# Performance work log

Measured on AMD Instinct MI355X. Metric: run time of the kernel, lower is better.

The kernel has to match this reference:

```python
import jax, jax.numpy as jnp
import numpy as np

N_HEAD = 12
D_HEAD = 64  # key_dim // n_head = 768 // 12


def sparsemax(z):
    # Martins & Astudillo (2016): projection of each row of z onto the simplex.
    K = z.shape[-1]
    z_sorted = -jnp.sort(-z, axis=-1)                      # descending sort
    cs = jnp.cumsum(z_sorted, axis=-1)
    r = jnp.arange(1, K + 1, dtype=z.dtype)
    support = (1.0 + r * z_sorted) > cs                    # support set indicator
    ksz = jnp.sum(support, axis=-1, keepdims=True)         # support size k(z)
    cs_k = jnp.take_along_axis(cs, ksz.astype(jnp.int32) - 1, axis=-1)
    tau = (cs_k - 1.0) / ksz.astype(z.dtype)               # threshold
    return jnp.maximum(z - tau, 0.0)


def setup_inputs() -> dict:
    key = jax.random.key(0)
    kq, kk, kv, kwq, kbq, kwk, kbk = jax.random.split(key, 7)
    B, L, D = 8, 1024, 768
    scale = 0.02
    return {
        "q": jax.random.normal(kq, (B, L, D), jnp.float32),
        "k": jax.random.normal(kk, (B, L, D), jnp.float32),
        "v": jax.random.normal(kv, (B, L, D), jnp.float32),
        "Wq": jax.random.normal(kwq, (D, D), jnp.float32) * scale,  # torch Linear weight [out,in]
        "bq": jax.random.normal(kbq, (D,), jnp.float32) * scale,
        "Wk": jax.random.normal(kwk, (D, D), jnp.float32) * scale,
        "bk": jax.random.normal(kbk, (D,), jnp.float32) * scale,
    }


def reference(q, k, v, Wq, bq, Wk, bk):
    B, Lq, _ = q.shape
    Lkv = k.shape[1]
    # project and split heads: [B, H, L, d_head]
    qh = (q @ Wq.T + bq).reshape(B, Lq, N_HEAD, D_HEAD).transpose(0, 2, 1, 3)
    kh = (k @ Wk.T + bk).reshape(B, Lkv, N_HEAD, D_HEAD).transpose(0, 2, 1, 3)
    inv_sqrt_d = jnp.asarray(1.0 / np.sqrt(D_HEAD), q.dtype)
    scores = jnp.einsum("bhqd,bhkd->bhqk", qh, kh) * inv_sqrt_d  # [B,H,Lq,Lkv]
    attn = sparsemax(scores)
    attn = attn.mean(axis=1)                                      # head-mean -> [B,Lq,Lkv]
    # eval mode: smooth_max is identity (training-only smoothing)
    output = jnp.einsum("bqk,bkd->bqd", attn, v)                  # [B,Lq,Dv]
    return output, attn
```

## Files before the change

kernel.cpp:

```cpp
#include <hip/hip_runtime.h>

#define BSZ 8
#define NH 12
#define LSEQ 1024
#define DMODEL 768
#define DHEAD 64
#define OUT_ELEMS 6291456
#define ATTN_ELEMS 8388608

typedef __attribute__((ext_vector_type(8))) short short8;
typedef __attribute__((ext_vector_type(4))) float f32x4;

__device__ __forceinline__ int   f2i(float x) { union { float f; int i; } c; c.f = x; return c.i; }
__device__ __forceinline__ float i2f(int x)   { union { int i; float f; } c; c.i = x; return c.f; }

__device__ __forceinline__ unsigned short f2bf(float x) {
    union { float f; unsigned u; } c; c.f = x;
    unsigned r = (c.u + 0x7FFF + ((c.u >> 16) & 1)) >> 16;
    return (unsigned short)r;
}
__device__ __forceinline__ float bf2f(unsigned short h) {
    union { float f; unsigned u; } c; c.u = ((unsigned)h) << 16;
    return c.f;
}
__device__ __forceinline__ void split2(float x, unsigned short& h, unsigned short& l) {
    h = f2bf(x);
    l = f2bf(x - bf2f(h));
}

template<int CTRL>
__device__ __forceinline__ float dppadd(float v) {
    return v + i2f(__builtin_amdgcn_update_dpp(0, f2i(v), CTRL, 0xF, 0xF, true));
}
template<int CTRL>
__device__ __forceinline__ float dppmax(float v) {
    return fmaxf(v, i2f(__builtin_amdgcn_update_dpp(f2i(v), f2i(v), CTRL, 0xF, 0xF, false)));
}

__device__ __forceinline__ void wsum2(float s[2]) {
#define WS(CTRL) _Pragma("unroll") for (int rr = 0; rr < 2; ++rr) { s[rr] = dppadd<CTRL>(s[rr]); }
    WS(0x111) WS(0x112) WS(0x114) WS(0x118) WS(0x142) WS(0x143)
#undef WS
#pragma unroll
    for (int rr = 0; rr < 2; ++rr) s[rr] = i2f(__builtin_amdgcn_readlane(f2i(s[rr]), 63));
}

__device__ __forceinline__ void wred6(float s[2], float q[2], float m[2]) {
#define WS(CTRL) _Pragma("unroll") for (int rr = 0; rr < 2; ++rr) { s[rr] = dppadd<CTRL>(s[rr]); q[rr] = dppadd<CTRL>(q[rr]); m[rr] = dppmax<CTRL>(m[rr]); }
    WS(0x111) WS(0x112) WS(0x114) WS(0x118) WS(0x142) WS(0x143)
#undef WS
#pragma unroll
    for (int rr = 0; rr < 2; ++rr) {
        s[rr] = i2f(__builtin_amdgcn_readlane(f2i(s[rr]), 63));
        q[rr] = i2f(__builtin_amdgcn_readlane(f2i(q[rr]), 63));
        m[rr] = i2f(__builtin_amdgcn_readlane(f2i(m[rr]), 63));
    }
}

__global__ __launch_bounds__(256) void proj_mfma(
    const float* __restrict__ qin, const float* __restrict__ kin,
    const float* __restrict__ Wq, const float* __restrict__ bq,
    const float* __restrict__ Wk, const float* __restrict__ bk,
    unsigned short* __restrict__ ws) {
    const float* A; const float* W; const float* bias;
    unsigned short* hi; unsigned short* lo;
    if (blockIdx.z == 0) { A = qin; W = Wq; bias = bq; hi = ws;                lo = ws + OUT_ELEMS; }
    else                 { A = kin; W = Wk; bias = bk; hi = ws + 2*OUT_ELEMS; lo = ws + 3*OUT_ELEMS; }

    __shared__ unsigned short Ah[128][32], Al[128][32];
    __shared__ unsigned short Bh[128][32], Bl[128][32];

    const int t    = threadIdx.x;
    const int lane = t & 63;
    const int w    = t >> 6;
    const int wr   = w >> 1, wc = w & 1;
    const int mrow = lane & 15, quad = lane >> 4;
    const int m0   = blockIdx.y * 128;
    const int n0   = blockIdx.x * 128;

    const int srow = t >> 3;
    const int scol = (t & 7) * 4;

    f32x4 acc[4][4];
#pragma unroll
    for (int i = 0; i < 4; ++i)
#pragma unroll
        for (int j = 0; j < 4; ++j) acc[i][j] = (f32x4){0.f, 0.f, 0.f, 0.f};

    for (int k0 = 0; k0 < DMODEL; k0 += 32) {
        float4 av[4], wv[4];
#pragma unroll
        for (int i = 0; i < 4; ++i) {
            av[i] = *(const float4*)&A[(size_t)(m0 + srow + i * 32) * DMODEL + k0 + scol];
            wv[i] = *(const float4*)&W[(size_t)(n0 + srow + i * 32) * DMODEL + k0 + scol];
        }
        __syncthreads();
#pragma unroll
        for (int i = 0; i < 4; ++i) {
            ushort4 h4, l4;
            split2(av[i].x, h4.x, l4.x); split2(av[i].y, h4.y, l4.y);
            split2(av[i].z, h4.z, l4.z); split2(av[i].w, h4.w, l4.w);
            *(ushort4*)&Ah[srow + i * 32][scol] = h4;
            *(ushort4*)&Al[srow + i * 32][scol] = l4;
            split2(wv[i].x, h4.x, l4.x); split2(wv[i].y, h4.y, l4.y);
            split2(wv[i].z, h4.z, l4.z); split2(wv[i].w, h4.w, l4.w);
            *(ushort4*)&Bh[srow + i * 32][scol] = h4;
            *(ushort4*)&Bl[srow + i * 32][scol] = l4;
        }
        __syncthreads();

        short8 ah[4], al[4], bh[4], bl[4];
#pragma unroll
        for (int i = 0; i < 4; ++i) {
            ah[i] = *(const short8*)&Ah[wr * 64 + i * 16 + mrow][quad * 8];
            al[i] = *(const short8*)&Al[wr * 64 + i * 16 + mrow][quad * 8];
            bh[i] = *(const short8*)&Bh[wc * 64 + i * 16 + mrow][quad * 8];
            bl[i] = *(const short8*)&Bl[wc * 64 + i * 16 + mrow][quad * 8];
        }
#pragma unroll
        for (int i = 0; i < 4; ++i)
#pragma unroll
            for (int j = 0; j < 4; ++j) {
                acc[i][j] = __builtin_amdgcn_mfma_f32_16x16x32_bf16(al[i], bh[j], acc[i][j], 0, 0, 0);
                acc[i][j] = __builtin_amdgcn_mfma_f32_16x16x32_bf16(ah[i], bl[j], acc[i][j], 0, 0, 0);
                acc[i][j] = __builtin_amdgcn_mfma_f32_16x16x32_bf16(ah[i], bh[j], acc[i][j], 0, 0, 0);
            }
    }

#pragma unroll
    for (int j = 0; j < 4; ++j) {
        const int ng = n0 + wc * 64 + j * 16 + mrow;
        const float bj = bias[ng];
        const int hh = ng >> 6, dd = ng & 63;
#pragma unroll
        for (int i = 0; i < 4; ++i) {
#pragma unroll
            for (int reg = 0; reg < 4; ++reg) {
                const int mg = m0 + wr * 64 + i * 16 + quad * 4 + reg;
                const float c = acc[i][j][reg] + bj;
                unsigned short ch, cl;
                split2(c, ch, cl);
                const size_t idx = (((size_t)(mg >> 10) * NH + hh) * LSEQ + (mg & 1023)) * DHEAD + dd;
                hi[idx] = ch;
                lo[idx] = cl;
            }
        }
    }
}

__global__ __launch_bounds__(512, 4) void attn_kernel(
    const unsigned short* __restrict__ ws, float* __restrict__ attn_out) {
    __shared__ float S[16 * 1024];

    const unsigned short* Qhi = ws;
    const unsigned short* Qlo = ws + OUT_ELEMS;
    const unsigned short* Khi = ws + 2 * OUT_ELEMS;
    const unsigned short* Klo = ws + 3 * OUT_ELEMS;

    const int t = threadIdx.x;
    const int lane = t & 63;
    const int w = t >> 6;
    const int idlin = blockIdx.x + 64 * blockIdx.y;
    const int b  = idlin & 7;
    const int q0 = (idlin >> 3) * 16;
    const int hoff = ((idlin >> 3) & 1) * 6;

    const int mrow = lane & 15;
    const int quad = lane >> 4;

    float macc[2][16];
#pragma unroll
    for (int rr = 0; rr < 2; ++rr)
#pragma unroll
        for (int j = 0; j < 16; ++j) macc[rr][j] = 0.f;

    size_t hb;
    short8 qh0, qh1, ql0, ql1;
    short8 kah0, kah1, kal0, kal1;
    short8 kbh0, kbh1, kbl0, kbl1;
    short8 kch0, kch1, kcl0, kcl1;

#define QLOAD() do { \
    const size_t aoff_ = hb + (size_t)(q0 + mrow) * DHEAD + quad * 8; \
    qh0 = *(const short8*)(Qhi + aoff_); \
    qh1 = *(const short8*)(Qhi + aoff_ + 32); \
    ql0 = *(const short8*)(Qlo + aoff_); \
    ql1 = *(const short8*)(Qlo + aoff_ + 32); \
} while (0)

#define KLOAD(P, nt) do { \
    const size_t boff_ = hb + (size_t)(w * 128 + (nt) * 16 + mrow) * DHEAD + quad * 8; \
    P##h0 = *(const short8*)(Khi + boff_); \
    P##h1 = *(const short8*)(Khi + boff_ + 32); \
    P##l0 = *(const short8*)(Klo + boff_); \
    P##l1 = *(const short8*)(Klo + boff_ + 32); \
} while (0)

#define KMFMA(P, nt) do { \
    f32x4 d_ = (f32x4){0.f, 0.f, 0.f, 0.f}; \
    d_ = __builtin_amdgcn_mfma_f32_16x16x32_bf16(ql0, P##h0, d_, 0, 0, 0); \
    d_ = __builtin_amdgcn_mfma_f32_16x16x32_bf16(qh0, P##l0, d_, 0, 0, 0); \
    d_ = __builtin_amdgcn_mfma_f32_16x16x32_bf16(qh0, P##h0, d_, 0, 0, 0); \
    d_ = __builtin_amdgcn_mfma_f32_16x16x32_bf16(ql1, P##h1, d_, 0, 0, 0); \
    d_ = __builtin_amdgcn_mfma_f32_16x16x32_bf16(qh1, P##l1, d_, 0, 0, 0); \
    d_ = __builtin_amdgcn_mfma_f32_16x16x32_bf16(qh1, P##h1, d_, 0, 0, 0); \
    const int swcol_ = (w * 128 + (nt) * 16 + mrow) ^ (quad << 4); \
    _Pragma("unroll") for (int reg = 0; reg < 4; ++reg) \
        S[(quad * 4 + reg) * 1024 + swcol_] = d_[reg] * 0.125f; \
} while (0)

#define SP_PASS() do { \
    _Pragma("unroll") for (int rr = 0; rr < 2; ++rr) { \
        float a0 = 0.f, a1 = 0.f, a2 = 0.f, a3 = 0.f; \
        int c = 0; \
        _Pragma("unroll") for (int j = 0; j < 16; j += 4) { \
            bool g0 = z[rr][j]     > tau[rr]; \
            bool g1 = z[rr][j + 1] > tau[rr]; \
            bool g2 = z[rr][j + 2] > tau[rr]; \
            bool g3 = z[rr][j + 3] > tau[rr]; \
            c += __popcll(__ballot(g0)) + __popcll(__ballot(g1)) \
               + __popcll(__ballot(g2)) + __popcll(__ballot(g3)); \
            a0 += g0 ? z[rr][j]     : 0.f; \
            a1 += g1 ? z[rr][j + 1] : 0.f; \
            a2 += g2 ? z[rr][j + 2] : 0.f; \
            a3 += g3 ? z[rr][j + 3] : 0.f; \
        } \
        sI[rr] = (a0 + a1) + (a2 + a3); \
        cI[rr] = c; \
    } \
    wsum2(sI); \
} while (0)

    hb = ((size_t)b * NH + hoff) * (LSEQ * DHEAD);
    QLOAD();

#pragma unroll 1
    for (int i = 0; i < NH; ++i) {
        __syncthreads();

        KLOAD(ka, 0); KLOAD(kb, 1);
        KLOAD(kc, 2); KMFMA(ka, 0);
        KLOAD(ka, 3); KMFMA(kb, 1);
        KLOAD(kb, 4); KMFMA(kc, 2);
        KLOAD(kc, 5); KMFMA(ka, 3);
        KLOAD(ka, 6); KMFMA(kb, 4);
        KLOAD(kb, 7); KMFMA(kc, 5);
        KMFMA(ka, 6); KMFMA(kb, 7);
        __syncthreads();

        float z[2][16];
#pragma unroll
        for (int rr = 0; rr < 2; ++rr) {
            const int r = w * 2 + rr;
            const int swz = (r >> 2) << 4;
#pragma unroll
            for (int c = 0; c < 4; ++c)
                *(f32x4*)&z[rr][c * 4] = *(const f32x4*)&S[r * 1024 + ((c * 256 + lane * 4) ^ swz)];
        }

        if (i + 1 < NH) {
            int hn = i + 1 + hoff; if (hn >= NH) hn -= NH;
            hb = ((size_t)b * NH + hn) * (LSEQ * DHEAD);
            QLOAD();
        }

        float sv[2], qv[2], mv[2];
#pragma unroll
        for (int rr = 0; rr < 2; ++rr) {
            float s0 = 0.f, s1 = 0.f, s2 = 0.f, s3 = 0.f;
            float p0 = 0.f, p1 = 0.f, p2 = 0.f, p3 = 0.f;
            float m0 = z[rr][0], m1 = z[rr][1], m2 = z[rr][2], m3 = z[rr][3];
#pragma unroll
            for (int j = 0; j < 16; j += 4) {
                s0 += z[rr][j]; s1 += z[rr][j + 1]; s2 += z[rr][j + 2]; s3 += z[rr][j + 3];
                p0 = fmaf(z[rr][j],     z[rr][j],     p0);
                p1 = fmaf(z[rr][j + 1], z[rr][j + 1], p1);
                p2 = fmaf(z[rr][j + 2], z[rr][j + 2], p2);
                p3 = fmaf(z[rr][j + 3], z[rr][j + 3], p3);
            }
#pragma unroll
            for (int j = 4; j < 16; j += 4) {
                m0 = fmaxf(m0, z[rr][j]);     m1 = fmaxf(m1, z[rr][j + 1]);
                m2 = fmaxf(m2, z[rr][j + 2]); m3 = fmaxf(m3, z[rr][j + 3]);
            }
            sv[rr] = (s0 + s1) + (s2 + s3);
            qv[rr] = (p0 + p1) + (p2 + p3);
            mv[rr] = fmaxf(fmaxf(m0, m1), fmaxf(m2, m3));
        }
        wred6(sv, qv, mv);

        float tau[2], t0s[2]; int prev[2]; bool done[2];
#pragma unroll
        for (int rr = 0; rr < 2; ++rr) {
            t0s[rr] = fmaxf((sv[rr] - 1.0f) * (1.0f / 1024.0f), mv[rr] - 1.0f);
            const float mu  = sv[rr] * (1.0f / 1024.0f);
            const float var = fmaxf(qv[rr] * (1.0f / 1024.0f) - mu * mu, 1e-12f);
            const float sg  = sqrtf(var);
            const float a   = 2.7196f + 0.33333f * __logf(sg);
            const float tg  = mu + (a - 0.25f) * sg;
            tau[rr] = fminf(fmaxf(tg, t0s[rr]), mv[rr] - 1e-3f);
            prev[rr] = -1; done[rr] = false;
        }

        {
            float sI[2]; int cI[2];
            SP_PASS();
#pragma unroll
            for (int rr = 0; rr < 2; ++rr) {
                const float tn = (sI[rr] - 1.0f) / (float)cI[rr];
                if (tn >= tau[rr]) { tau[rr] = tn; prev[rr] = cI[rr]; }
                else               { tau[rr] = t0s[rr]; }
            }
        }

        for (int it = 0; it < 63; ++it) {
            float sI[2]; int cI[2];
            SP_PASS();
            bool alldone = true;
#pragma unroll
            for (int rr = 0; rr < 2; ++rr) {
                if (!done[rr]) {
                    if (cI[rr] == prev[rr]) done[rr] = true;
                    else { tau[rr] = (sI[rr] - 1.0f) / (float)cI[rr]; prev[rr] = cI[rr]; }
                }
                alldone = alldone && done[rr];
            }
            if (alldone) break;
        }

#pragma unroll
        for (int rr = 0; rr < 2; ++rr)
#pragma unroll
            for (int j = 0; j < 16; ++j)
                macc[rr][j] += fmaxf(z[rr][j] - tau[rr], 0.f);
    }

    float* ao = attn_out + ((size_t)b * LSEQ + q0) * LSEQ;
#pragma unroll
    for (int rr = 0; rr < 2; ++rr) {
        const int r = w * 2 + rr;
#pragma unroll
        for (int c = 0; c < 4; ++c) {
            f32x4 o;
#pragma unroll
            for (int j = 0; j < 4; ++j) o[j] = macc[rr][c * 4 + j] * (1.0f / 12.0f);
            *(f32x4*)&ao[(size_t)r * LSEQ + c * 256 + lane * 4] = o;
        }
    }
#undef QLOAD
#undef KLOAD
#undef KMFMA
#undef SP_PASS
}

__global__ __launch_bounds__(256) void out_mfma(
    const float* __restrict__ attn, const float* __restrict__ v,
    float* __restrict__ out) {
    const int b = blockIdx.z;
    const float* Ab = attn + (size_t)b * LSEQ * LSEQ;
    const float* Vb = v    + (size_t)b * LSEQ * DMODEL;
    float* Cb       = out  + (size_t)b * LSEQ * DMODEL;

    __shared__ unsigned short Ah[128][32], Al[128][32];
    __shared__ unsigned short Bh[128][36], Bl[128][36];

    const int t    = threadIdx.x;
    const int lane = t & 63;
    const int w    = t >> 6;
    const int wr   = w >> 1, wc = w & 1;
    const int mrow = lane & 15, quad = lane >> 4;
    const int m0   = blockIdx.y * 128;
    const int n0   = blockIdx.x * 128;

    const int srow = t >> 3;
    const int scol = (t & 7) * 4;
    const int bn   = t & 127;
    const int bk0  = (t >> 7) * 16;

    f32x4 acc[4][4];
#pragma unroll
    for (int i = 0; i < 4; ++i)
#pragma unroll
        for (int j = 0; j < 4; ++j) acc[i][j] = (f32x4){0.f, 0.f, 0.f, 0.f};

    for (int k0 = 0; k0 < LSEQ; k0 += 32) {
        float4 av[4];
#pragma unroll
        for (int i = 0; i < 4; ++i)
            av[i] = *(const float4*)&Ab[(size_t)(m0 + srow + i * 32) * LSEQ + k0 + scol];
        float bv[16];
#pragma unroll
        for (int i = 0; i < 16; ++i)
            bv[i] = Vb[(size_t)(k0 + bk0 + i) * DMODEL + n0 + bn];

        __syncthreads();
#pragma unroll
        for (int i = 0; i < 4; ++i) {
            ushort4 h4, l4;
            split2(av[i].x, h4.x, l4.x); split2(av[i].y, h4.y, l4.y);
            split2(av[i].z, h4.z, l4.z); split2(av[i].w, h4.w, l4.w);
            *(ushort4*)&Ah[srow + i * 32][scol] = h4;
            *(ushort4*)&Al[srow + i * 32][scol] = l4;
        }
#pragma unroll
        for (int g = 0; g < 4; ++g) {
            ushort4 h4, l4;
            split2(bv[g * 4 + 0], h4.x, l4.x); split2(bv[g * 4 + 1], h4.y, l4.y);
            split2(bv[g * 4 + 2], h4.z, l4.z); split2(bv[g * 4 + 3], h4.w, l4.w);
            *(ushort4*)&Bh[bn][bk0 + g * 4] = h4;
            *(ushort4*)&Bl[bn][bk0 + g * 4] = l4;
        }
        __syncthreads();

        short8 ah[4], al[4], bh[4], bl[4];
#pragma unroll
        for (int i = 0; i < 4; ++i) {
            ah[i] = *(const short8*)&Ah[wr * 64 + i * 16 + mrow][quad * 8];
            al[i] = *(const short8*)&Al[wr * 64 + i * 16 + mrow][quad * 8];
        }
#pragma unroll
        for (int j = 0; j < 4; ++j) {
            const unsigned short* ph = &Bh[wc * 64 + j * 16 + mrow][quad * 8];
            const unsigned short* pl = &Bl[wc * 64 + j * 16 + mrow][quad * 8];
            uint2 h0 = *(const uint2*)ph;
            uint2 h1 = *(const uint2*)(ph + 4);
            uint2 l0 = *(const uint2*)pl;
            uint2 l1 = *(const uint2*)(pl + 4);
            union { uint u[4]; short8 s; } ch, cl;
            ch.u[0] = h0.x; ch.u[1] = h0.y; ch.u[2] = h1.x; ch.u[3] = h1.y;
            cl.u[0] = l0.x; cl.u[1] = l0.y; cl.u[2] = l1.x; cl.u[3] = l1.y;
            bh[j] = ch.s; bl[j] = cl.s;
        }
#pragma unroll
        for (int i = 0; i < 4; ++i)
#pragma unroll
            for (int j = 0; j < 4; ++j) {
                acc[i][j] = __builtin_amdgcn_mfma_f32_16x16x32_bf16(al[i], bh[j], acc[i][j], 0, 0, 0);
                acc[i][j] = __builtin_amdgcn_mfma_f32_16x16x32_bf16(ah[i], bl[j], acc[i][j], 0, 0, 0);
                acc[i][j] = __builtin_amdgcn_mfma_f32_16x16x32_bf16(ah[i], bh[j], acc[i][j], 0, 0, 0);
            }
    }

#pragma unroll
    for (int i = 0; i < 4; ++i)
#pragma unroll
        for (int j = 0; j < 4; ++j)
#pragma unroll
            for (int reg = 0; reg < 4; ++reg) {
                const int mg = m0 + wr * 64 + i * 16 + quad * 4 + reg;
                const int ng = n0 + wc * 64 + j * 16 + mrow;
                Cb[(size_t)mg * DMODEL + ng] = acc[i][j][reg];
            }
}

extern "C" void kernel_launch(void* const* d_in, const int* in_sizes, int n_in,
                              void* d_out, int out_size, void* d_ws, size_t ws_size,
                              hipStream_t stream) {
    const float* q  = (const float*)d_in[0];
    const float* k  = (const float*)d_in[1];
    const float* v  = (const float*)d_in[2];
    const float* Wq = (const float*)d_in[3];
    const float* bq = (const float*)d_in[4];
    const float* Wk = (const float*)d_in[5];
    const float* bk = (const float*)d_in[6];

    float* out  = (float*)d_out;
    float* attn = out + OUT_ELEMS;
    unsigned short* ws = (unsigned short*)d_ws;

    hipLaunchKernelGGL(proj_mfma, dim3(6, 64, 2), dim3(256), 0, stream,
                       q, k, Wq, bq, Wk, bk, ws);
    hipLaunchKernelGGL(attn_kernel, dim3(64, 8), dim3(512), 0, stream,
                       ws, attn);
    hipLaunchKernelGGL(out_mfma, dim3(6, 8, 8), dim3(256), 0, stream,
                       attn, v, out);
}
```

Measured before the change: 526.1 us.

## Overlap next-head QK MFMA with sparsemax by splitting warps into two phases

```diff
diff --git a/kernel.cpp b/kernel.cpp
--- a/kernel.cpp
+++ b/kernel.cpp
@@ -176,9 +176,7 @@
 
     size_t hb;
     short8 qh0, qh1, ql0, ql1;
-    short8 kah0, kah1, kal0, kal1;
-    short8 kbh0, kbh1, kbl0, kbl1;
-    short8 kch0, kch1, kcl0, kcl1;
+    short8 kh0, kh1, kl0, kl1;
 
 #define QLOAD() do { \
     const size_t aoff_ = hb + (size_t)(q0 + mrow) * DHEAD + quad * 8; \
@@ -188,25 +186,32 @@
     ql1 = *(const short8*)(Qlo + aoff_ + 32); \
 } while (0)
 
-#define KLOAD(P, nt) do { \
+#define KLOAD(nt) do { \
     const size_t boff_ = hb + (size_t)(w * 128 + (nt) * 16 + mrow) * DHEAD + quad * 8; \
-    P##h0 = *(const short8*)(Khi + boff_); \
-    P##h1 = *(const short8*)(Khi + boff_ + 32); \
-    P##l0 = *(const short8*)(Klo + boff_); \
-    P##l1 = *(const short8*)(Klo + boff_ + 32); \
-} while (0)
-
-#define KMFMA(P, nt) do { \
+    kh0 = *(const short8*)(Khi + boff_); \
+    kh1 = *(const short8*)(Khi + boff_ + 32); \
+    kl0 = *(const short8*)(Klo + boff_); \
+    kl1 = *(const short8*)(Klo + boff_ + 32); \
+} while (0)
+
+#define KMFMA(nt) do { \
     f32x4 d_ = (f32x4){0.f, 0.f, 0.f, 0.f}; \
-    d_ = __builtin_amdgcn_mfma_f32_16x16x32_bf16(ql0, P##h0, d_, 0, 0, 0); \
-    d_ = __builtin_amdgcn_mfma_f32_16x16x32_bf16(qh0, P##l0, d_, 0, 0, 0); \
-    d_ = __builtin_amdgcn_mfma_f32_16x16x32_bf16(qh0, P##h0, d_, 0, 0, 0); \
-    d_ = __builtin_amdgcn_mfma_f32_16x16x32_bf16(ql1, P##h1, d_, 0, 0, 0); \
-    d_ = __builtin_amdgcn_mfma_f32_16x16x32_bf16(qh1, P##l1, d_, 0, 0, 0); \
-    d_ = __builtin_amdgcn_mfma_f32_16x16x32_bf16(qh1, P##h1, d_, 0, 0, 0); \
+    d_ = __builtin_amdgcn_mfma_f32_16x16x32_bf16(ql0, kh0, d_, 0, 0, 0); \
+    d_ = __builtin_amdgcn_mfma_f32_16x16x32_bf16(qh0, kl0, d_, 0, 0, 0); \
+    d_ = __builtin_amdgcn_mfma_f32_16x16x32_bf16(qh0, kh0, d_, 0, 0, 0); \
+    d_ = __builtin_amdgcn_mfma_f32_16x16x32_bf16(ql1, kh1, d_, 0, 0, 0); \
+    d_ = __builtin_amdgcn_mfma_f32_16x16x32_bf16(qh1, kl1, d_, 0, 0, 0); \
+    d_ = __builtin_amdgcn_mfma_f32_16x16x32_bf16(qh1, kh1, d_, 0, 0, 0); \
     const int swcol_ = (w * 128 + (nt) * 16 + mrow) ^ (quad << 4); \
     _Pragma("unroll") for (int reg = 0; reg < 4; ++reg) \
         S[(quad * 4 + reg) * 1024 + swcol_] = d_[reg] * 0.125f; \
+} while (0)
+
+#define QK_ALL() do { \
+    KLOAD(0); KMFMA(0); KLOAD(1); KMFMA(1); \
+    KLOAD(2); KMFMA(2); KLOAD(3); KMFMA(3); \
+    KLOAD(4); KMFMA(4); KLOAD(5); KMFMA(5); \
+    KLOAD(6); KMFMA(6); KLOAD(7); KMFMA(7); \
 } while (0)
 
 #define SP_PASS() do { \
@@ -231,21 +236,74 @@
     wsum2(sI); \
 } while (0)
 
+#define SPARSEMAX_MACC() do { \
+    float sv[2], qv[2], mv[2]; \
+    _Pragma("unroll") for (int rr = 0; rr < 2; ++rr) { \
+        float s0 = 0.f, s1 = 0.f, s2 = 0.f, s3 = 0.f; \
+        float p0 = 0.f, p1 = 0.f, p2 = 0.f, p3 = 0.f; \
+        float m0 = z[rr][0], m1 = z[rr][1], m2 = z[rr][2], m3 = z[rr][3]; \
+        _Pragma("unroll") for (int j = 0; j < 16; j += 4) { \
+            s0 += z[rr][j]; s1 += z[rr][j + 1]; s2 += z[rr][j + 2]; s3 += z[rr][j + 3]; \
+            p0 = fmaf(z[rr][j],     z[rr][j],     p0); \
+            p1 = fmaf(z[rr][j + 1], z[rr][j + 1], p1); \
+            p2 = fmaf(z[rr][j + 2], z[rr][j + 2], p2); \
+            p3 = fmaf(z[rr][j + 3], z[rr][j + 3], p3); \
+        } \
+        _Pragma("unroll") for (int j = 4; j < 16; j += 4) { \
+            m0 = fmaxf(m0, z[rr][j]);     m1 = fmaxf(m1, z[rr][j + 1]); \
+            m2 = fmaxf(m2, z[rr][j + 2]); m3 = fmaxf(m3, z[rr][j + 3]); \
+        } \
+        sv[rr] = (s0 + s1) + (s2 + s3); \
+        qv[rr] = (p0 + p1) + (p2 + p3); \
+        mv[rr] = fmaxf(fmaxf(m0, m1), fmaxf(m2, m3)); \
+    } \
+    wred6(sv, qv, mv); \
+    float tau[2], t0s[2]; int prev[2]; bool done[2]; \
+    _Pragma("unroll") for (int rr = 0; rr < 2; ++rr) { \
+        t0s[rr] = fmaxf((sv[rr] - 1.0f) * (1.0f / 1024.0f), mv[rr] - 1.0f); \
+        const float mu  = sv[rr] * (1.0f / 1024.0f); \
+        const float var = fmaxf(qv[rr] * (1.0f / 1024.0f) - mu * mu, 1e-12f); \
+        const float sg  = sqrtf(var); \
+        const float a   = 2.7196f + 0.33333f * __logf(sg); \
+        const float tg  = mu + (a - 0.25f) * sg; \
+        tau[rr] = fminf(fmaxf(tg, t0s[rr]), mv[rr] - 1e-3f); \
+        prev[rr] = -1; done[rr] = false; \
+    } \
+    { \
+        float sI[2]; int cI[2]; \
+        SP_PASS(); \
+        _Pragma("unroll") for (int rr = 0; rr < 2; ++rr) { \
+            const float tn = (sI[rr] - 1.0f) / (float)cI[rr]; \
+            if (tn >= tau[rr]) { tau[rr] = tn; prev[rr] = cI[rr]; } \
+            else               { tau[rr] = t0s[rr]; } \
+        } \
+    } \
+    for (int it = 0; it < 63; ++it) { \
+        float sI[2]; int cI[2]; \
+        SP_PASS(); \
+        bool alldone = true; \
+        _Pragma("unroll") for (int rr = 0; rr < 2; ++rr) { \
+            if (!done[rr]) { \
+                if (cI[rr] == prev[rr]) done[rr] = true; \
+                else { tau[rr] = (sI[rr] - 1.0f) / (float)cI[rr]; prev[rr] = cI[rr]; } \
+            } \
+            alldone = alldone && done[rr]; \
+        } \
+        if (alldone) break; \
+    } \
+    _Pragma("unroll") for (int rr = 0; rr < 2; ++rr) \
+        _Pragma("unroll") for (int j = 0; j < 16; ++j) \
+            macc[rr][j] += fmaxf(z[rr][j] - tau[rr], 0.f); \
+} while (0)
+
     hb = ((size_t)b * NH + hoff) * (LSEQ * DHEAD);
     QLOAD();
+    QK_ALL();
+
+    const bool qkFirst = (w >= 4);
 
 #pragma unroll 1
     for (int i = 0; i < NH; ++i) {
-        __syncthreads();
-
-        KLOAD(ka, 0); KLOAD(kb, 1);
-        KLOAD(kc, 2); KMFMA(ka, 0);
-        KLOAD(ka, 3); KMFMA(kb, 1);
-        KLOAD(kb, 4); KMFMA(kc, 2);
-        KLOAD(kc, 5); KMFMA(ka, 3);
-        KLOAD(ka, 6); KMFMA(kb, 4);
-        KLOAD(kb, 7); KMFMA(kc, 5);
-        KMFMA(ka, 6); KMFMA(kb, 7);
         __syncthreads();
 
         float z[2][16];
@@ -258,81 +316,20 @@
                 *(f32x4*)&z[rr][c * 4] = *(const f32x4*)&S[r * 1024 + ((c * 256 + lane * 4) ^ swz)];
         }
 
-        if (i + 1 < NH) {
+        const bool hasNext = (i + 1 < NH);
+        if (hasNext) {
             int hn = i + 1 + hoff; if (hn >= NH) hn -= NH;
             hb = ((size_t)b * NH + hn) * (LSEQ * DHEAD);
             QLOAD();
         }
 
-        float sv[2], qv[2], mv[2];
-#pragma unroll
-        for (int rr = 0; rr < 2; ++rr) {
-            float s0 = 0.f, s1 = 0.f, s2 = 0.f, s3 = 0.f;
-            float p0 = 0.f, p1 = 0.f, p2 = 0.f, p3 = 0.f;
-            float m0 = z[rr][0], m1 = z[rr][1], m2 = z[rr][2], m3 = z[rr][3];
-#pragma unroll
-            for (int j = 0; j < 16; j += 4) {
-                s0 += z[rr][j]; s1 += z[rr][j + 1]; s2 += z[rr][j + 2]; s3 += z[rr][j + 3];
-                p0 = fmaf(z[rr][j],     z[rr][j],     p0);
-                p1 = fmaf(z[rr][j + 1], z[rr][j + 1], p1);
-                p2 = fmaf(z[rr][j + 2], z[rr][j + 2], p2);
-                p3 = fmaf(z[rr][j + 3], z[rr][j + 3], p3);
-            }
-#pragma unroll
-            for (int j = 4; j < 16; j += 4) {
-                m0 = fmaxf(m0, z[rr][j]);     m1 = fmaxf(m1, z[rr][j + 1]);
-                m2 = fmaxf(m2, z[rr][j + 2]); m3 = fmaxf(m3, z[rr][j + 3]);
-            }
-            sv[rr] = (s0 + s1) + (s2 + s3);
-            qv[rr] = (p0 + p1) + (p2 + p3);
-            mv[rr] = fmaxf(fmaxf(m0, m1), fmaxf(m2, m3));
-        }
-        wred6(sv, qv, mv);
-
-        float tau[2], t0s[2]; int prev[2]; bool done[2];
-#pragma unroll
-        for (int rr = 0; rr < 2; ++rr) {
-            t0s[rr] = fmaxf((sv[rr] - 1.0f) * (1.0f / 1024.0f), mv[rr] - 1.0f);
-            const float mu  = sv[rr] * (1.0f / 1024.0f);
-            const float var = fmaxf(qv[rr] * (1.0f / 1024.0f) - mu * mu, 1e-12f);
-            const float sg  = sqrtf(var);
-            const float a   = 2.7196f + 0.33333f * __logf(sg);
-            const float tg  = mu + (a - 0.25f) * sg;
-            tau[rr] = fminf(fmaxf(tg, t0s[rr]), mv[rr] - 1e-3f);
-            prev[rr] = -1; done[rr] = false;
-        }
-
-        {
-            float sI[2]; int cI[2];
-            SP_PASS();
-#pragma unroll
-            for (int rr = 0; rr < 2; ++rr) {
-                const float tn = (sI[rr] - 1.0f) / (float)cI[rr];
-                if (tn >= tau[rr]) { tau[rr] = tn; prev[rr] = cI[rr]; }
-                else               { tau[rr] = t0s[rr]; }
-            }
-        }
-
-        for (int it = 0; it < 63; ++it) {
-            float sI[2]; int cI[2];
-            SP_PASS();
-            bool alldone = true;
-#pragma unroll
-            for (int rr = 0; rr < 2; ++rr) {
-                if (!done[rr]) {
-                    if (cI[rr] == prev[rr]) done[rr] = true;
-                    else { tau[rr] = (sI[rr] - 1.0f) / (float)cI[rr]; prev[rr] = cI[rr]; }
-                }
-                alldone = alldone && done[rr];
-            }
-            if (alldone) break;
-        }
-
-#pragma unroll
-        for (int rr = 0; rr < 2; ++rr)
-#pragma unroll
-            for (int j = 0; j < 16; ++j)
-                macc[rr][j] += fmaxf(z[rr][j] - tau[rr], 0.f);
+        __syncthreads();
+
+        if (qkFirst && hasNext) QK_ALL();
+
+        SPARSEMAX_MACC();
+
+        if (!qkFirst && hasNext) QK_ALL();
     }
 
     float* ao = attn_out + ((size_t)b * LSEQ + q0) * LSEQ;
@@ -350,7 +347,9 @@
 #undef QLOAD
 #undef KLOAD
 #undef KMFMA
+#undef QK_ALL
 #undef SP_PASS
+#undef SPARSEMAX_MACC
 }
 
 __global__ __launch_bounds__(256) void out_mfma(
```

New measurement: 521.4 us. About the same (-0.9%).
